# Performance work log

Measured on AMD Instinct MI355X. Metric: run time of the kernel, lower is better.

Reference implementation:

```python
import jax, jax.numpy as jnp
import numpy as np

DEPTH = 4
CHUNK = 16


def tp(a, b):
    """Graded tensor (outer) product on flattened levels: (...,m)x(...,n)->(...,m*n)."""
    return jnp.einsum('...i,...j->...ij', a, b).reshape(*a.shape[:-1], a.shape[-1] * b.shape[-1])


def ta_mul(a, b):
    """Truncated tensor-algebra product of two group-like elements (implicit level-0 == 1).
    a, b: lists of levels 1..D, level k flattened to C**k."""
    out = []
    for k in range(len(a)):
        t = a[k] + b[k]
        for i in range(k):
            t = t + tp(a[i], b[k - 1 - i])
        out.append(t)
    return out


def ta_mulz(a, b):
    """Product when both elements have level-0 == 0."""
    out = []
    for k in range(len(a)):
        t = jnp.zeros_like(a[k])
        for i in range(k):
            t = t + tp(a[i], b[k - 1 - i])
        out.append(t)
    return out


def ta_exp(a):
    """exp of a level-0-free element, truncated at DEPTH; returns levels 1..D (level-0 == 1 implicit)."""
    out = list(a)
    p = a
    fact = 1.0
    for m in range(2, len(a) + 1):
        p = ta_mulz(a, p)
        fact *= m
        out = [o + q / fact for o, q in zip(out, p)]
    return out


def ta_log(s):
    """Truncated log of group-like element g = 1 + s; input s = levels 1..D of g."""
    out = list(s)
    p = s
    sign = 1.0
    for m in range(2, len(s) + 1):
        p = ta_mulz(s, p)
        sign = -sign
        out = [o + (sign / m) * q for o, q in zip(out, p)]
    return out


def bch(a, b):
    """BCH merge: log(exp(a) (x) exp(b)) in the truncated algebra."""
    return ta_log(ta_mul(ta_exp(a), ta_exp(b)))


def exp_l1(d):
    """exp of a pure level-1 element d (shape (...,C)): level k = d^(x)k / k!."""
    levels = [d]
    cur = d
    fact = 1.0
    for k in range(2, DEPTH + 1):
        cur = tp(cur, d)
        fact *= k
        levels.append(cur / fact)
    return levels


def chunk_signatures(inc):
    """inc: (B, N, L, C) per-chunk increments -> signature levels [(B,N,C), (B,N,C^2), ...]
    via Chen: sig = exp(d_1) (x) ... (x) exp(d_L)."""
    carry0 = tuple(exp_l1(inc[:, :, 0]))
    xs = jnp.moveaxis(inc[:, :, 1:], 2, 0)  # (L-1, B, N, C)
    def step(carry, d):
        return tuple(ta_mul(list(carry), exp_l1(d))), None
    carry, _ = jax.lax.scan(step, carry0, xs)
    return list(carry)


def hillis_steele(levels):
    """Inclusive associative scan over chunk dim (axis=1) with BCH merge.
    bch(0, b) == b exactly, so zero-padding handles the boundary."""
    N = levels[0].shape[1]
    pref = levels
    d = 1
    while d < N:
        shifted = [jnp.concatenate([jnp.zeros_like(l[:, :d]), l[:, :-d]], axis=1) for l in pref]
        pref = bch(shifted, pref)
        d *= 2
    return pref


def _forward(x, W1, b1, W2, b2):
    B, T, Cin = x.shape
    t = jnp.linspace(0.0, 1.0, T, dtype=x.dtype)
    path = jnp.concatenate([x, jnp.broadcast_to(t[None, :, None], (B, T, 1)).astype(x.dtype)], axis=-1)
    C = Cin + 1
    # basepoint=True: path starts at 0, so increments are diff of [0; path]
    inc = jnp.diff(path, axis=1, prepend=jnp.zeros((B, 1, C), x.dtype))
    N = T // CHUNK
    inc = inc.reshape(B, N, CHUNK, C)
    sig = chunk_signatures(inc)          # levels 1..D, (B,N,C^k)
    logl = ta_log(sig)                   # truncated log-signature per chunk
    pref = hillis_steele(logl)           # inclusive BCH prefix scan
    flat = jnp.concatenate(pref, axis=-1)  # (B, N, mem_dim)
    pooled = flat.mean(axis=1)           # readout_pool == 'mean'
    h = jnp.maximum(pooled @ W1 + b1, 0.0)
    return h @ W2 + b2


def setup_inputs() -> dict:
    key = jax.random.key(0)
    k0, k1, k2 = jax.random.split(key, 3)
    B, T, Cin = 8, 2048, 7
    mem_dim, H, out_dim = 4680, 256, 1
    x = jax.random.normal(k0, (B, T, Cin), dtype=jnp.float32)
    W1 = jax.random.normal(k1, (mem_dim, H), dtype=jnp.float32) * (1.0 / np.sqrt(mem_dim))
    b1 = jnp.zeros((H,), jnp.float32)
    W2 = jax.random.normal(k2, (H, out_dim), dtype=jnp.float32) * (1.0 / np.sqrt(H))
    b2 = jnp.zeros((out_dim,), jnp.float32)
    return {"x": x, "W1": W1, "b1": b1, "W2": W2, "b2": b2}


def reference(x, W1, b1, W2, b2):
    return _forward(x, W1, b1, W2, b2)
```

## Files before the change

kernel.cpp:

```cpp
#include <hip/hip_runtime.h>


#define MEM   4680
#define NG    32
#define TLEN  2048

#define P3OFF 72
#define P4OFF 648
#define SIGSZ 5256

__device__ __forceinline__ void load_inc(const float* __restrict__ x, int b, int g,
                                         float* sInc, int tid) {
    for (int e = tid; e < 512; e += 256) {
        int s = e >> 3, c = e & 7;
        int t = g * 64 + s;
        float v;
        if (c < 7) {
            float cur  = x[(b * TLEN + t) * 7 + c];
            float prev = (t > 0) ? x[(b * TLEN + t - 1) * 7 + c] : 0.f;
            v = cur - prev;
        } else v = (t > 0) ? (1.f / 2047.f) : 0.f;
        sInc[e] = v;
    }
}

__device__ __forceinline__ void chunk_step(const float* dch, float* sA, float* U, int tid) {
    float* loc3 = U;
    float* loc2 = U + 576;
    float* loc1 = U + 640;
    const int i1 = tid >> 6, j1 = (tid >> 3) & 7, k1 = tid & 7;
    const int row1 = tid >> 3, row2 = row1 + 32;
    const int jk = tid & 63;
    const int pos2 = tid + 256, i2 = pos2 >> 6;
    float p1a = 0.f, l2a = 0.f, l3a = 0.f, p1b = 0.f, l2b = 0.f, l3b = 0.f;
    float Sa[8], Sb[8];
#pragma unroll
    for (int l = 0; l < 8; l++) { Sa[l] = 0.f; Sb[l] = 0.f; }
#pragma unroll
    for (int t = 0; t < 16; t++) {
        const float* dr = dch + t * 8;
        float di1 = dr[i1], di2 = dr[i2], dj = dr[j1], dk = dr[k1];
        float ga = l3a + dk * (l2a * 0.5f + dj * (p1a * (1.f/6.f) + di1 * (1.f/24.f)));
        float gb = l3b + dk * (l2b * 0.5f + dj * (p1b * (1.f/6.f) + di2 * (1.f/24.f)));
#pragma unroll
        for (int l = 0; l < 8; l++) { float dv = dr[l]; Sa[l] += ga * dv; Sb[l] += gb * dv; }
        l3a += dk * (l2a + dj * (p1a * 0.5f + di1 * (1.f/6.f)));
        l3b += dk * (l2b + dj * (p1b * 0.5f + di2 * (1.f/6.f)));
        l2a += (p1a + di1 * 0.5f) * dj;
        l2b += (p1b + di2 * 0.5f) * dj;
        p1a += di1; p1b += di2;
    }
    loc3[row1 * 9 + k1] = l3a;
    loc3[row2 * 9 + k1] = l3b;
    if (k1 == 0) { loc2[row1] = l2a; loc2[row2] = l2b; }
    if (jk == 0) { loc1[i1] = p1a; loc1[i2] = p1b; }
    __syncthreads();
    float a1 = sA[i1], a2 = sA[8 + row1], a3 = sA[P3OFF + row1 * 9 + k1];
    float c1_ = sA[i2], c2_ = sA[8 + row2], c3_ = sA[P3OFF + row2 * 9 + k1];
    const float* l3p = &loc3[jk * 9];
    const float* l2p = &loc2[k1 * 8];
    float n4a[8], n4b[8];
#pragma unroll
    for (int l = 0; l < 8; l++) {
        float v3 = l3p[l], v2 = l2p[l], v1 = loc1[l];
        n4a[l] = sA[P4OFF + tid * 9 + l]  + Sa[l] + a1 * v3 + a2 * v2 + a3 * v1;
        n4b[l] = sA[P4OFF + pos2 * 9 + l] + Sb[l] + c1_ * v3 + c2_ * v2 + c3_ * v1;
    }
    float n3a = a3 + l3a + a1 * loc2[jk] + a2 * loc1[k1];
    float n3b = c3_ + l3b + c1_ * loc2[jk] + c2_ * loc1[k1];
    float n2v = 0.f, n1v = 0.f;
    if (tid < 64) n2v = sA[8 + tid] + loc2[tid] + sA[tid >> 3] * loc1[tid & 7];
    if (tid < 8)  n1v = sA[tid] + loc1[tid];
    __syncthreads();
#pragma unroll
    for (int l = 0; l < 8; l++) { sA[P4OFF + tid * 9 + l] = n4a[l]; sA[P4OFF + pos2 * 9 + l] = n4b[l]; }
    sA[P3OFF + row1 * 9 + k1] = n3a;
    sA[P3OFF + row2 * 9 + k1] = n3b;
    if (tid < 64) sA[8 + tid] = n2v;
    if (tid < 8)  sA[tid] = n1v;
    __syncthreads();
}

__global__ __launch_bounds__(256) void sig_totals_kernel(const float* __restrict__ x,
                                                         float* __restrict__ T) {
    int blk = blockIdx.x;
    int b = blk >> 5, g = blk & 31;
    int tid = threadIdx.x;

    __shared__ __attribute__((aligned(16))) float sInc[512];
    __shared__ __attribute__((aligned(16))) float sA[SIGSZ];
    __shared__ __attribute__((aligned(16))) float U[648];

    load_inc(x, b, g, sInc, tid);
    for (int m = tid; m < SIGSZ; m += 256) sA[m] = 0.f;
    __syncthreads();
    for (int c = 0; c < 4; c++) chunk_step(&sInc[c * 128], sA, U, tid);

    size_t base = (size_t)blk * MEM;
    for (int m = tid; m < MEM; m += 256) {
        float v;
        if (m < 72) v = sA[m];
        else if (m < 584) { int e = m - 72;  v = sA[P3OFF + (e >> 3) * 9 + (e & 7)]; }
        else              { int e = m - 584; v = sA[P4OFF + (e >> 3) * 9 + (e & 7)]; }
        T[base + m] = v;
    }
}

__global__ __launch_bounds__(256) void scan_fused_kernel(const float* __restrict__ T,
                                                         float* __restrict__ P) {
    int bx = blockIdx.x;
    int b = bx >> 4, s = bx & 15;
    int tid = threadIdx.x;

    __shared__ float st1[NG][8];
    __shared__ float st2[NG][64];
    __shared__ float st3[NG][32];
    __shared__ float sp1[NG][8];
    __shared__ float sp2[NG][64];
    __shared__ float sp3[NG][32];

    int bBase = b * NG;
    {
        int g = tid >> 3, i = tid & 7;
        st1[g][i] = T[(size_t)(bBase + g) * MEM + i];
    }
    for (int m = tid; m < NG * 64; m += 256) {
        int g = m >> 6, e = m & 63;
        st2[g][e] = T[(size_t)(bBase + g) * MEM + 8 + e];
    }
    for (int m = tid; m < NG * 32; m += 256) {
        int g = m >> 5, e = m & 31;
        st3[g][e] = T[(size_t)(bBase + g) * MEM + 72 + s * 32 + e];
    }
    __syncthreads();

    if (tid < 64) {
        int i = tid >> 3, k = tid & 7;
        float p1acc = 0.f, p2acc = 0.f;
        for (int g = 0; g < NG; g++) {
            sp2[g][tid] = p2acc;
            if (k == 0) sp1[g][i] = p1acc;
            if (s == 0) {
                size_t prow = (size_t)(bBase + g) * MEM;
                P[prow + 8 + tid] = p2acc;
                if (k == 0) P[prow + i] = p1acc;
            }
            p2acc += st2[g][tid] + p1acc * st1[g][k];
            p1acc += st1[g][i];
        }
    }
    __syncthreads();
    if (tid < 32) {
        int ijk = s * 32 + tid;
        int i = ijk >> 6, jk = ijk & 63, ij = ijk >> 3, k = ijk & 7;
        float acc3 = 0.f;
        for (int g = 0; g < NG; g++) {
            sp3[g][tid] = acc3;
            P[(size_t)(bBase + g) * MEM + 72 + ijk] = acc3;
            acc3 += st3[g][tid] + sp1[g][i] * st2[g][jk] + sp2[g][ij] * st1[g][k];
        }
    }
    __syncthreads();
    {
        int m = s * 256 + tid;
        int i = m >> 9, jkl = m & 511, ij = m >> 6, kl = m & 63, l = m & 7;
        int p3loc = tid >> 3;
        float acc4 = 0.f;
#pragma unroll 4
        for (int g = 0; g < NG; g++) {
            size_t row = (size_t)(bBase + g) * MEM;
            P[row + 584 + m] = acc4;
            acc4 += T[row + 584 + m]
                  + sp1[g][i] * T[row + 72 + jkl]
                  + sp2[g][ij] * st2[g][kl]
                  + sp3[g][p3loc] * st1[g][l];
        }
    }
}

__global__ __launch_bounds__(256) void apply_log_pool_kernel(const float* __restrict__ x,
                                                             const float* __restrict__ P,
                                                             float* __restrict__ partial) {
    int blk = blockIdx.x;
    int b = blk >> 5, g = blk & 31;
    int tid = threadIdx.x;

    __shared__ __attribute__((aligned(16))) float sInc[512];
    __shared__ __attribute__((aligned(16))) float sA[SIGSZ];
    __shared__ __attribute__((aligned(16))) float sP[SIGSZ];
    __shared__ __attribute__((aligned(16))) float U[648];
    __shared__ __attribute__((aligned(16))) float sR[648];
    __shared__ __attribute__((aligned(16))) float sQ23[576];

    load_inc(x, b, g, sInc, tid);
    {
        size_t base = (size_t)blk * MEM;
        if (tid < 72) sP[tid] = P[base + tid];
        for (int e = tid; e < 512; e += 256)
            sP[P3OFF + (e >> 3) * 9 + (e & 7)] = P[base + 72 + e];
        for (int e = tid; e < 4096; e += 256)
            sP[P4OFF + (e >> 3) * 9 + (e & 7)] = P[base + 584 + e];
    }
    for (int m = tid; m < SIGSZ; m += 256) sA[m] = 0.f;
    __syncthreads();

    const int i1 = tid >> 6, j1 = (tid >> 3) & 7, k1 = tid & 7;
    const int row1 = tid >> 3, row2 = row1 + 32;
    const int jk = tid & 63;
    const int pos2 = tid + 256, i2 = pos2 >> 6;

    float pool4a[8], pool4b[8];
#pragma unroll
    for (int l = 0; l < 8; l++) { pool4a[l] = 0.f; pool4b[l] = 0.f; }
    float pool3a = 0.f, pool3b = 0.f, pool2 = 0.f, pool1 = 0.f;

    for (int c = 0; c < 4; c++) {
        chunk_step(&sInc[c * 128], sA, U, tid);

        float a1 = sP[i1], a2 = sP[8 + row1], a3 = sP[P3OFF + row1 * 9 + k1];
        float c1_ = sP[i2], c2_ = sP[8 + row2], c3_ = sP[P3OFF + row2 * 9 + k1];
        const float* q3p = &sA[P3OFF + jk * 9];
        const float* q2p = &sA[8 + k1 * 8];
        float R4a[8], R4b[8];
#pragma unroll
        for (int l = 0; l < 8; l++) {
            float v3 = q3p[l], v2 = q2p[l], v1 = sA[l];
            R4a[l] = sP[P4OFF + tid * 9 + l]  + sA[P4OFF + tid * 9 + l]  + a1 * v3 + a2 * v2 + a3 * v1;
            R4b[l] = sP[P4OFF + pos2 * 9 + l] + sA[P4OFF + pos2 * 9 + l] + c1_ * v3 + c2_ * v2 + c3_ * v1;
        }
        float R3a = a3 + sA[P3OFF + row1 * 9 + k1] + a1 * sA[8 + jk] + a2 * sA[k1];
        float R3b = c3_ + sA[P3OFF + row2 * 9 + k1] + c1_ * sA[8 + jk] + c2_ * sA[k1];
        float R2v = 0.f, R1v = 0.f;
        if (tid < 64) R2v = sP[8 + tid] + sA[8 + tid] + sP[tid >> 3] * sA[tid & 7];
        if (tid < 8)  R1v = sP[tid] + sA[tid];

        sR[P3OFF + row1 * 9 + k1] = R3a;
        sR[P3OFF + row2 * 9 + k1] = R3b;
        if (tid < 64) sR[8 + tid] = R2v;
        if (tid < 8)  sR[tid] = R1v;
        __syncthreads();

        float q23a = sR[i1] * sR[8 + jk] + sR[8 + row1] * sR[k1];
        float q23b = sR[i2] * sR[8 + jk] + sR[8 + row2] * sR[k1];
        sQ23[row1 * 9 + k1] = q23a;
        sQ23[row2 * 9 + k1] = q23b;
        __syncthreads();

        {
            float s1ia = sR[i1], s1ib = sR[i2], s1j = sR[j1], s1k = sR[k1];
            float s2ija = sR[8 + row1], s2ijb = sR[8 + row2];
            const float* r3p = &sR[P3OFF + jk * 9];
            const float* r2p = &sR[8 + k1 * 8];
            const float* q23p = &sQ23[jk * 9];
#pragma unroll
            for (int l = 0; l < 8; l++) {
                float s1l = sR[l];
                float p22 = s1k * s1l;
                float p24a = s1ia * r3p[l] + s2ija * r2p[l] + R3a * s1l;
                float p24b = s1ib * r3p[l] + s2ijb * r2p[l] + R3b * s1l;
                float p34a = s1ia * q23p[l] + s2ija * p22;
                float p34b = s1ib * q23p[l] + s2ijb * p22;
                float p44a = s1ia * s1j * p22;
                float p44b = s1ib * s1j * p22;
                pool4a[l] += R4a[l] - 0.5f * p24a + (1.f/3.f) * p34a - 0.25f * p44a;
                pool4b[l] += R4b[l] - 0.5f * p24b + (1.f/3.f) * p34b - 0.25f * p44b;
            }
            pool3a += R3a - 0.5f * q23a + (1.f/3.f) * s1ia * s1j * s1k;
            pool3b += R3b - 0.5f * q23b + (1.f/3.f) * s1ib * s1j * s1k;
            if (tid < 64) pool2 += R2v - 0.5f * sR[tid >> 3] * sR[tid & 7];
            if (tid < 8)  pool1 += R1v;
        }
        __syncthreads();
    }

    {
        float* pb = partial + (size_t)blk * MEM;
        float4 va0 = make_float4(pool4a[0], pool4a[1], pool4a[2], pool4a[3]);
        float4 va1 = make_float4(pool4a[4], pool4a[5], pool4a[6], pool4a[7]);
        float4 vb0 = make_float4(pool4b[0], pool4b[1], pool4b[2], pool4b[3]);
        float4 vb1 = make_float4(pool4b[4], pool4b[5], pool4b[6], pool4b[7]);
        float4* d1 = (float4*)(pb + 584 + tid * 8);
        d1[0] = va0; d1[1] = va1;
        float4* d2 = (float4*)(pb + 584 + (tid + 256) * 8);
        d2[0] = vb0; d2[1] = vb1;
        pb[72 + tid] = pool3a;
        pb[72 + tid + 256] = pool3b;
        if (tid < 64) pb[8 + tid] = pool2;
        if (tid < 8)  pb[tid] = pool1;
    }
}

__global__ __launch_bounds__(256) void gemv1_kernel(const float* __restrict__ partial,
                                                    const float* __restrict__ W1,
                                                    float* __restrict__ hpart) {
    int kc = blockIdx.x;
    int tid = threadIdx.x;
    int k0 = kc * 32;
    __shared__ float sp[8][32];
    {
        int b = tid >> 5, k = tid & 31;
        float sum = 0.f;
        if (k0 + k < MEM) {
            for (int g = 0; g < NG; g++)
                sum += partial[(size_t)(b * NG + g) * MEM + k0 + k];
        }
        sp[b][k] = sum * (1.f / 128.f);
    }
    __syncthreads();
    float acc[8];
#pragma unroll
    for (int b = 0; b < 8; b++) acc[b] = 0.f;
    int kend = (k0 + 32 < MEM) ? 32 : (MEM - k0);
    for (int k = 0; k < kend; k++) {
        float wv = W1[(size_t)(k0 + k) * 256 + tid];
#pragma unroll
        for (int b = 0; b < 8; b++) acc[b] += sp[b][k] * wv;
    }
#pragma unroll
    for (int b = 0; b < 8; b++) hpart[(size_t)kc * 2048 + b * 256 + tid] = acc[b];
}

__global__ __launch_bounds__(256) void final_kernel(const float* __restrict__ hpart,
                                                    const float* __restrict__ b1,
                                                    const float* __restrict__ W2,
                                                    const float* __restrict__ b2,
                                                    float* __restrict__ outp) {
    int b = blockIdx.x;
    int tid = threadIdx.x;
    float v = 0.f;
    for (int kc = 0; kc < 147; kc++) v += hpart[(size_t)kc * 2048 + b * 256 + tid];
    v += b1[tid];
    v = fmaxf(v, 0.f) * W2[tid];
    __shared__ float sRed[256];
    sRed[tid] = v;
    __syncthreads();
    for (int s = 128; s > 0; s >>= 1) {
        if (tid < s) sRed[tid] += sRed[tid + s];
        __syncthreads();
    }
    if (tid == 0) outp[b] = sRed[0] + b2[0];
}

extern "C" void kernel_launch(void* const* d_in, const int* in_sizes, int n_in,
                              void* d_out, int out_size, void* d_ws, size_t ws_size,
                              hipStream_t stream) {
    const float* x  = (const float*)d_in[0];
    const float* W1 = (const float*)d_in[1];
    const float* b1 = (const float*)d_in[2];
    const float* W2 = (const float*)d_in[3];
    const float* b2 = (const float*)d_in[4];
    float* out = (float*)d_out;

    float* ws = (float*)d_ws;
    float* T       = ws;
    float* P       = T + (size_t)256 * MEM;
    float* partial = P + (size_t)256 * MEM;
    float* hpart   = partial + (size_t)256 * MEM;

    sig_totals_kernel<<<256, 256, 0, stream>>>(x, T);
    scan_fused_kernel<<<128, 256, 0, stream>>>(T, P);
    apply_log_pool_kernel<<<256, 256, 0, stream>>>(x, P, partial);
    gemv1_kernel<<<147, 256, 0, stream>>>(partial, W1, hpart);
    final_kernel<<<8, 256, 0, stream>>>(hpart, b1, W2, b2, out);
}
```

Measured before the change: 126.8 us.

## Use 512 threads per block, one level-4 row per thread, skip first Chen merge

The signature and log-pool kernels now launch 512 threads per block, and each thread handles one level-4 row instead of two. This halves per-thread registers and serial work and doubles the waves available per CU, so latency is better hidden across the 256-block grid. The first chunk writes its local signature straight into the accumulator instead of merging with zeros, which drops a zero-init pass and one combine step. A small unroll pragma is added to the gemv partial reduction. Bigger blocks mean more barrier cost per sync.

Result: slower. 161.8 us (+27.7%).

```diff
diff --git a/kernel.cpp b/kernel.cpp
--- a/kernel.cpp
+++ b/kernel.cpp
@@ -4,100 +4,109 @@
 #define MEM   4680
 #define NG    32
 #define TLEN  2048
-
 #define P3OFF 72
 #define P4OFF 648
 #define SIGSZ 5256
 
-__device__ __forceinline__ void load_inc(const float* __restrict__ x, int b, int g,
-                                         float* sInc, int tid) {
-    for (int e = tid; e < 512; e += 256) {
-        int s = e >> 3, c = e & 7;
-        int t = g * 64 + s;
-        float v;
-        if (c < 7) {
-            float cur  = x[(b * TLEN + t) * 7 + c];
-            float prev = (t > 0) ? x[(b * TLEN + t - 1) * 7 + c] : 0.f;
-            v = cur - prev;
-        } else v = (t > 0) ? (1.f / 2047.f) : 0.f;
-        sInc[e] = v;
-    }
+__device__ __forceinline__ void load_padded512(float* dst, const float* __restrict__ src, int tid) {
+    if (tid < 72) dst[tid] = src[tid];
+    if (tid < 512) dst[P3OFF + (tid >> 3) * 9 + (tid & 7)] = src[72 + tid];
+    for (int e = tid; e < 4096; e += 512) dst[P4OFF + (e >> 3) * 9 + (e & 7)] = src[584 + e];
+}
+
+__device__ __forceinline__ void load_inc512(const float* __restrict__ x, int b, int g,
+                                            float* sInc, int tid) {
+    int s = tid >> 3, c = tid & 7;
+    int t = g * 64 + s;
+    float v;
+    if (c < 7) {
+        float cur  = x[(b * TLEN + t) * 7 + c];
+        float prev = (t > 0) ? x[(b * TLEN + t - 1) * 7 + c] : 0.f;
+        v = cur - prev;
+    } else v = (t > 0) ? (1.f / 2047.f) : 0.f;
+    sInc[tid] = v;
+}
+
+#define CHUNK_RECUR(dch)                                                            \
+    float p1 = 0.f, l2 = 0.f, l3 = 0.f;                                             \
+    float S[8];                                                                     \
+    _Pragma("unroll")                                                               \
+    for (int l = 0; l < 8; l++) S[l] = 0.f;                                         \
+    _Pragma("unroll")                                                               \
+    for (int t = 0; t < 16; t++) {                                                  \
+        const float* dr = (dch) + t * 8;                                            \
+        float di = dr[i], dj = dr[j], dk = dr[k];                                   \
+        float gg = l3 + dk * (l2 * 0.5f + dj * (p1 * (1.f/6.f) + di * (1.f/24.f))); \
+        _Pragma("unroll")                                                           \
+        for (int l = 0; l < 8; l++) S[l] += gg * dr[l];                             \
+        l3 += dk * (l2 + dj * (p1 * 0.5f + di * (1.f/6.f)));                        \
+        l2 += (p1 + di * 0.5f) * dj;                                                \
+        p1 += di;                                                                   \
+    }
+
+__device__ __forceinline__ void chunk_step_first(const float* dch, float* sA, int tid) {
+    const int i = tid >> 6, j = (tid >> 3) & 7, k = tid & 7;
+    const int row = tid >> 3, jk = tid & 63;
+    CHUNK_RECUR(dch)
+#pragma unroll
+    for (int l = 0; l < 8; l++) sA[P4OFF + tid * 9 + l] = S[l];
+    sA[P3OFF + row * 9 + k] = l3;
+    if (k == 0) sA[8 + row] = l2;
+    if (jk == 0) sA[i] = p1;
+    __syncthreads();
+    (void)j;
 }
 
 __device__ __forceinline__ void chunk_step(const float* dch, float* sA, float* U, int tid) {
     float* loc3 = U;
     float* loc2 = U + 576;
     float* loc1 = U + 640;
-    const int i1 = tid >> 6, j1 = (tid >> 3) & 7, k1 = tid & 7;
-    const int row1 = tid >> 3, row2 = row1 + 32;
-    const int jk = tid & 63;
-    const int pos2 = tid + 256, i2 = pos2 >> 6;
-    float p1a = 0.f, l2a = 0.f, l3a = 0.f, p1b = 0.f, l2b = 0.f, l3b = 0.f;
-    float Sa[8], Sb[8];
-#pragma unroll
-    for (int l = 0; l < 8; l++) { Sa[l] = 0.f; Sb[l] = 0.f; }
-#pragma unroll
-    for (int t = 0; t < 16; t++) {
-        const float* dr = dch + t * 8;
-        float di1 = dr[i1], di2 = dr[i2], dj = dr[j1], dk = dr[k1];
-        float ga = l3a + dk * (l2a * 0.5f + dj * (p1a * (1.f/6.f) + di1 * (1.f/24.f)));
-        float gb = l3b + dk * (l2b * 0.5f + dj * (p1b * (1.f/6.f) + di2 * (1.f/24.f)));
-#pragma unroll
-        for (int l = 0; l < 8; l++) { float dv = dr[l]; Sa[l] += ga * dv; Sb[l] += gb * dv; }
-        l3a += dk * (l2a + dj * (p1a * 0.5f + di1 * (1.f/6.f)));
-        l3b += dk * (l2b + dj * (p1b * 0.5f + di2 * (1.f/6.f)));
-        l2a += (p1a + di1 * 0.5f) * dj;
-        l2b += (p1b + di2 * 0.5f) * dj;
-        p1a += di1; p1b += di2;
-    }
-    loc3[row1 * 9 + k1] = l3a;
-    loc3[row2 * 9 + k1] = l3b;
-    if (k1 == 0) { loc2[row1] = l2a; loc2[row2] = l2b; }
-    if (jk == 0) { loc1[i1] = p1a; loc1[i2] = p1b; }
-    __syncthreads();
-    float a1 = sA[i1], a2 = sA[8 + row1], a3 = sA[P3OFF + row1 * 9 + k1];
-    float c1_ = sA[i2], c2_ = sA[8 + row2], c3_ = sA[P3OFF + row2 * 9 + k1];
+    const int i = tid >> 6, j = (tid >> 3) & 7, k = tid & 7;
+    const int row = tid >> 3, jk = tid & 63;
+    CHUNK_RECUR(dch)
+    loc3[row * 9 + k] = l3;
+    if (k == 0) loc2[row] = l2;
+    if (jk == 0) loc1[i] = p1;
+    __syncthreads();
+    float a1 = sA[i], a2 = sA[8 + row], a3 = sA[P3OFF + row * 9 + k];
     const float* l3p = &loc3[jk * 9];
-    const float* l2p = &loc2[k1 * 8];
-    float n4a[8], n4b[8];
-#pragma unroll
-    for (int l = 0; l < 8; l++) {
-        float v3 = l3p[l], v2 = l2p[l], v1 = loc1[l];
-        n4a[l] = sA[P4OFF + tid * 9 + l]  + Sa[l] + a1 * v3 + a2 * v2 + a3 * v1;
-        n4b[l] = sA[P4OFF + pos2 * 9 + l] + Sb[l] + c1_ * v3 + c2_ * v2 + c3_ * v1;
-    }
-    float n3a = a3 + l3a + a1 * loc2[jk] + a2 * loc1[k1];
-    float n3b = c3_ + l3b + c1_ * loc2[jk] + c2_ * loc1[k1];
+    const float* l2p = &loc2[k * 8];
+    float n4[8];
+#pragma unroll
+    for (int l = 0; l < 8; l++)
+        n4[l] = sA[P4OFF + tid * 9 + l] + S[l] + a1 * l3p[l] + a2 * l2p[l] + a3 * loc1[l];
+    float n3 = a3 + l3 + a1 * loc2[jk] + a2 * loc1[k];
     float n2v = 0.f, n1v = 0.f;
     if (tid < 64) n2v = sA[8 + tid] + loc2[tid] + sA[tid >> 3] * loc1[tid & 7];
     if (tid < 8)  n1v = sA[tid] + loc1[tid];
     __syncthreads();
 #pragma unroll
-    for (int l = 0; l < 8; l++) { sA[P4OFF + tid * 9 + l] = n4a[l]; sA[P4OFF + pos2 * 9 + l] = n4b[l]; }
-    sA[P3OFF + row1 * 9 + k1] = n3a;
-    sA[P3OFF + row2 * 9 + k1] = n3b;
+    for (int l = 0; l < 8; l++) sA[P4OFF + tid * 9 + l] = n4[l];
+    sA[P3OFF + row * 9 + k] = n3;
     if (tid < 64) sA[8 + tid] = n2v;
     if (tid < 8)  sA[tid] = n1v;
     __syncthreads();
-}
-
-__global__ __launch_bounds__(256) void sig_totals_kernel(const float* __restrict__ x,
+    (void)j;
+}
+
+__global__ __launch_bounds__(512) void sig_totals_kernel(const float* __restrict__ x,
                                                          float* __restrict__ T) {
     int blk = blockIdx.x;
     int b = blk >> 5, g = blk & 31;
     int tid = threadIdx.x;
-
     __shared__ __attribute__((aligned(16))) float sInc[512];
     __shared__ __attribute__((aligned(16))) float sA[SIGSZ];
     __shared__ __attribute__((aligned(16))) float U[648];
 
-    load_inc(x, b, g, sInc, tid);
-    for (int m = tid; m < SIGSZ; m += 256) sA[m] = 0.f;
-    __syncthreads();
-    for (int c = 0; c < 4; c++) chunk_step(&sInc[c * 128], sA, U, tid);
+    load_inc512(x, b, g, sInc, tid);
+    __syncthreads();
+    chunk_step_first(&sInc[0], sA, tid);
+    chunk_step(&sInc[128], sA, U, tid);
+    chunk_step(&sInc[256], sA, U, tid);
+    chunk_step(&sInc[384], sA, U, tid);
 
     size_t base = (size_t)blk * MEM;
-    for (int m = tid; m < MEM; m += 256) {
+    for (int m = tid; m < MEM; m += 512) {
         float v;
         if (m < 72) v = sA[m];
         else if (m < 584) { int e = m - 72;  v = sA[P3OFF + (e >> 3) * 9 + (e & 7)]; }
@@ -178,7 +187,7 @@
     }
 }
 
-__global__ __launch_bounds__(256) void apply_log_pool_kernel(const float* __restrict__ x,
+__global__ __launch_bounds__(512) void apply_log_pool_kernel(const float* __restrict__ x,
                                                              const float* __restrict__ P,
                                                              float* __restrict__ partial) {
     int blk = blockIdx.x;
@@ -192,81 +201,60 @@
     __shared__ __attribute__((aligned(16))) float sR[648];
     __shared__ __attribute__((aligned(16))) float sQ23[576];
 
-    load_inc(x, b, g, sInc, tid);
-    {
-        size_t base = (size_t)blk * MEM;
-        if (tid < 72) sP[tid] = P[base + tid];
-        for (int e = tid; e < 512; e += 256)
-            sP[P3OFF + (e >> 3) * 9 + (e & 7)] = P[base + 72 + e];
-        for (int e = tid; e < 4096; e += 256)
-            sP[P4OFF + (e >> 3) * 9 + (e & 7)] = P[base + 584 + e];
-    }
-    for (int m = tid; m < SIGSZ; m += 256) sA[m] = 0.f;
-    __syncthreads();
-
-    const int i1 = tid >> 6, j1 = (tid >> 3) & 7, k1 = tid & 7;
-    const int row1 = tid >> 3, row2 = row1 + 32;
-    const int jk = tid & 63;
-    const int pos2 = tid + 256, i2 = pos2 >> 6;
-
-    float pool4a[8], pool4b[8];
-#pragma unroll
-    for (int l = 0; l < 8; l++) { pool4a[l] = 0.f; pool4b[l] = 0.f; }
-    float pool3a = 0.f, pool3b = 0.f, pool2 = 0.f, pool1 = 0.f;
+    load_inc512(x, b, g, sInc, tid);
+    load_padded512(sP, P + (size_t)blk * MEM, tid);
+    __syncthreads();
+
+    const int i = tid >> 6, j = (tid >> 3) & 7, k = tid & 7;
+    const int row = tid >> 3, jk = tid & 63;
+
+    float pool4[8];
+#pragma unroll
+    for (int l = 0; l < 8; l++) pool4[l] = 0.f;
+    float pool3 = 0.f, pool2 = 0.f, pool1 = 0.f;
 
     for (int c = 0; c < 4; c++) {
-        chunk_step(&sInc[c * 128], sA, U, tid);
-
-        float a1 = sP[i1], a2 = sP[8 + row1], a3 = sP[P3OFF + row1 * 9 + k1];
-        float c1_ = sP[i2], c2_ = sP[8 + row2], c3_ = sP[P3OFF + row2 * 9 + k1];
-        const float* q3p = &sA[P3OFF + jk * 9];
-        const float* q2p = &sA[8 + k1 * 8];
-        float R4a[8], R4b[8];
-#pragma unroll
-        for (int l = 0; l < 8; l++) {
-            float v3 = q3p[l], v2 = q2p[l], v1 = sA[l];
-            R4a[l] = sP[P4OFF + tid * 9 + l]  + sA[P4OFF + tid * 9 + l]  + a1 * v3 + a2 * v2 + a3 * v1;
-            R4b[l] = sP[P4OFF + pos2 * 9 + l] + sA[P4OFF + pos2 * 9 + l] + c1_ * v3 + c2_ * v2 + c3_ * v1;
-        }
-        float R3a = a3 + sA[P3OFF + row1 * 9 + k1] + a1 * sA[8 + jk] + a2 * sA[k1];
-        float R3b = c3_ + sA[P3OFF + row2 * 9 + k1] + c1_ * sA[8 + jk] + c2_ * sA[k1];
+        if (c == 0) chunk_step_first(&sInc[0], sA, tid);
+        else        chunk_step(&sInc[c * 128], sA, U, tid);
+
+        float a1 = sP[i], a2 = sP[8 + row], a3 = sP[P3OFF + row * 9 + k];
+        const float* b3p = &sA[P3OFF + jk * 9];
+        const float* b2p = &sA[8 + k * 8];
+        float R4[8];
+#pragma unroll
+        for (int l = 0; l < 8; l++)
+            R4[l] = sP[P4OFF + tid * 9 + l] + sA[P4OFF + tid * 9 + l]
+                  + a1 * b3p[l] + a2 * b2p[l] + a3 * sA[l];
+        float R3 = a3 + sA[P3OFF + row * 9 + k] + a1 * sA[8 + jk] + a2 * sA[k];
         float R2v = 0.f, R1v = 0.f;
         if (tid < 64) R2v = sP[8 + tid] + sA[8 + tid] + sP[tid >> 3] * sA[tid & 7];
         if (tid < 8)  R1v = sP[tid] + sA[tid];
 
-        sR[P3OFF + row1 * 9 + k1] = R3a;
-        sR[P3OFF + row2 * 9 + k1] = R3b;
+        sR[P3OFF + row * 9 + k] = R3;
         if (tid < 64) sR[8 + tid] = R2v;
         if (tid < 8)  sR[tid] = R1v;
         __syncthreads();
 
-        float q23a = sR[i1] * sR[8 + jk] + sR[8 + row1] * sR[k1];
-        float q23b = sR[i2] * sR[8 + jk] + sR[8 + row2] * sR[k1];
-        sQ23[row1 * 9 + k1] = q23a;
-        sQ23[row2 * 9 + k1] = q23b;
+        float q23 = sR[i] * sR[8 + jk] + sR[8 + row] * sR[k];
+        sQ23[row * 9 + k] = q23;
         __syncthreads();
 
         {
-            float s1ia = sR[i1], s1ib = sR[i2], s1j = sR[j1], s1k = sR[k1];
-            float s2ija = sR[8 + row1], s2ijb = sR[8 + row2];
+            float s1i = sR[i], s1j = sR[j], s1k = sR[k];
+            float s2ij = sR[8 + row];
             const float* r3p = &sR[P3OFF + jk * 9];
-            const float* r2p = &sR[8 + k1 * 8];
+            const float* r2p = &sR[8 + k * 8];
             const float* q23p = &sQ23[jk * 9];
 #pragma unroll
             for (int l = 0; l < 8; l++) {
                 float s1l = sR[l];
                 float p22 = s1k * s1l;
-                float p24a = s1ia * r3p[l] + s2ija * r2p[l] + R3a * s1l;
-                float p24b = s1ib * r3p[l] + s2ijb * r2p[l] + R3b * s1l;
-                float p34a = s1ia * q23p[l] + s2ija * p22;
-                float p34b = s1ib * q23p[l] + s2ijb * p22;
-                float p44a = s1ia * s1j * p22;
-                float p44b = s1ib * s1j * p22;
-                pool4a[l] += R4a[l] - 0.5f * p24a + (1.f/3.f) * p34a - 0.25f * p44a;
-                pool4b[l] += R4b[l] - 0.5f * p24b + (1.f/3.f) * p34b - 0.25f * p44b;
+                float p24 = s1i * r3p[l] + s2ij * r2p[l] + R3 * s1l;
+                float p34 = s1i * q23p[l] + s2ij * p22;
+                float p44 = s1i * s1j * p22;
+                pool4[l] += R4[l] - 0.5f * p24 + (1.f/3.f) * p34 - 0.25f * p44;
             }
-            pool3a += R3a - 0.5f * q23a + (1.f/3.f) * s1ia * s1j * s1k;
-            pool3b += R3b - 0.5f * q23b + (1.f/3.f) * s1ib * s1j * s1k;
+            pool3 += R3 - 0.5f * q23 + (1.f/3.f) * s1i * s1j * s1k;
             if (tid < 64) pool2 += R2v - 0.5f * sR[tid >> 3] * sR[tid & 7];
             if (tid < 8)  pool1 += R1v;
         }
@@ -275,16 +263,10 @@
 
     {
         float* pb = partial + (size_t)blk * MEM;
-        float4 va0 = make_float4(pool4a[0], pool4a[1], pool4a[2], pool4a[3]);
-        float4 va1 = make_float4(pool4a[4], pool4a[5], pool4a[6], pool4a[7]);
-        float4 vb0 = make_float4(pool4b[0], pool4b[1], pool4b[2], pool4b[3]);
-        float4 vb1 = make_float4(pool4b[4], pool4b[5], pool4b[6], pool4b[7]);
         float4* d1 = (float4*)(pb + 584 + tid * 8);
-        d1[0] = va0; d1[1] = va1;
-        float4* d2 = (float4*)(pb + 584 + (tid + 256) * 8);
-        d2[0] = vb0; d2[1] = vb1;
-        pb[72 + tid] = pool3a;
-        pb[72 + tid + 256] = pool3b;
+        d1[0] = make_float4(pool4[0], pool4[1], pool4[2], pool4[3]);
+        d1[1] = make_float4(pool4[4], pool4[5], pool4[6], pool4[7]);
+        pb[72 + tid] = pool3;
         if (tid < 64) pb[8 + tid] = pool2;
         if (tid < 8)  pb[tid] = pool1;
     }
@@ -301,6 +283,7 @@
         int b = tid >> 5, k = tid & 31;
         float sum = 0.f;
         if (k0 + k < MEM) {
+#pragma unroll 4
             for (int g = 0; g < NG; g++)
                 sum += partial[(size_t)(b * NG + g) * MEM + k0 + k];
         }
@@ -357,9 +340,9 @@
     float* partial = P + (size_t)256 * MEM;
     float* hpart   = partial + (size_t)256 * MEM;
 
-    sig_totals_kernel<<<256, 256, 0, stream>>>(x, T);
+    sig_totals_kernel<<<256, 512, 0, stream>>>(x, T);
     scan_fused_kernel<<<128, 256, 0, stream>>>(T, P);
-    apply_log_pool_kernel<<<256, 256, 0, stream>>>(x, P, partial);
+    apply_log_pool_kernel<<<256, 512, 0, stream>>>(x, P, partial);
     gemv1_kernel<<<147, 256, 0, stream>>>(partial, W1, hpart);
     final_kernel<<<8, 256, 0, stream>>>(hpart, b1, W2, b2, out);
 }
```
